# Kernel tuning notes

Measured on AMD Instinct MI355X. Metric: run time of the kernel, lower is better.

Reference implementation:

```python
import jax, jax.numpy as jnp
import numpy as np

NUM_AA, EMB_DIM = 20, 16
H1, H2 = 128, 128
K, EXCLUDE = 64, 3
R_ON, R_CUT = 10.0, 12.0
RBF_CENTERS = (5.0, 6.0, 7.0, 8.0, 9.0, 10.0, 11.0)
RBF_WIDTH = 0.5
M = len(RBF_CENTERS)


def setup_inputs() -> dict:
    key = jax.random.key(0)
    ks = jax.random.split(key, 10)
    B, L = 8, 2048
    R = jax.random.normal(ks[0], (B, L, 3), dtype=jnp.float32) * 10.0  # spread distances over RBF range
    seq = jax.random.randint(ks[1], (B, L), 0, NUM_AA)
    emb_table = jax.random.normal(ks[2], (NUM_AA, EMB_DIM), dtype=jnp.float32) * 0.1
    in_dim = 3 * EMB_DIM
    W1 = jax.random.normal(ks[3], (in_dim, H1), dtype=jnp.float32) / np.sqrt(in_dim)
    b1 = jnp.zeros((H1,), jnp.float32)
    W2 = jax.random.normal(ks[4], (H1, H2), dtype=jnp.float32) / np.sqrt(H1)
    b2 = jnp.zeros((H2,), jnp.float32)
    W3 = jax.random.normal(ks[5], (H2, M), dtype=jnp.float32) / np.sqrt(H2)
    b3 = jnp.zeros((M,), jnp.float32)
    centers = jnp.asarray(RBF_CENTERS, jnp.float32)
    widths = jnp.full((M,), RBF_WIDTH, jnp.float32)
    return {"R": R, "seq": seq, "emb_table": emb_table,
            "W1": W1, "b1": b1, "W2": W2, "b2": b2, "W3": W3, "b3": b3,
            "centers": centers, "widths": widths}


def topk_nonbonded_pairs(R, K, exclude):
    # R: (B, L, 3) -> r: (B, L, K) distances, j: (B, L, K) neighbor indices
    B, L, _ = R.shape
    diff = R[:, :, None, :] - R[:, None, :, :]            # (B, L, L, 3)
    D = jnp.sqrt(jnp.sum(diff * diff, axis=-1) + 1e-12)   # (B, L, L)
    idx = jnp.arange(L)
    bonded = jnp.abs(idx[:, None] - idx[None, :]) <= exclude  # excludes self too
    D = jnp.where(bonded[None], jnp.inf, D)
    neg, j = jax.lax.top_k(-D, K)                          # K smallest distances
    return -neg, j


def smooth_switch(r, r_on, r_cut):
    t = jnp.clip((r - r_on) / (r_cut - r_on), 0.0, 1.0)
    return 1.0 - t * t * (3.0 - 2.0 * t)  # smoothstep down: 1 below r_on, 0 above r_cut


def distance_features(r, centers, widths):
    d = r[..., None] - centers  # (B, L, K, M)
    return jnp.exp(-(d * d) / (2.0 * widths * widths))


def reference(R, seq, emb_table, W1, b1, W2, b2, W3, b3, centers, widths):
    e = emb_table[seq]                                     # (B, L, d)
    r, j = topk_nonbonded_pairs(R, K, EXCLUDE)             # (B, L, K)
    e_j = jnp.take_along_axis(e[:, :, None, :], j[..., None], axis=1)  # wrong axis semantics avoided below
    # gather neighbor embeddings: e_j[b, i, k] = e[b, j[b, i, k]]
    e_j = jnp.take_along_axis(e[:, None, :, :].repeat(1, axis=1), j[..., None], axis=2) if False else \
          jnp.take_along_axis(e[:, :, None, :].transpose(0, 2, 1, 3).repeat(1, axis=0), j[..., None], axis=2) if False else \
          jax.vmap(lambda eb, jb: eb[jb])(e, j)            # (B, L, K, d)
    e_i = jnp.broadcast_to(e[:, :, None, :], e_j.shape)
    pair_feat = jnp.concatenate([e_i, e_j, e_i * e_j], axis=-1)  # (B, L, K, 3d)
    h = jax.nn.relu(pair_feat @ W1 + b1)
    h = jax.nn.relu(h @ W2 + b2)
    w = jax.nn.softplus(h @ W3 + b3)                       # (B, L, K, M)
    phi = distance_features(r, centers, widths)            # (B, L, K, M)
    att = -jnp.sum(w * phi, axis=-1)                       # (B, L, K)
    sw = smooth_switch(r, R_ON, R_CUT)
    return jnp.sum(att * sw, axis=(1, 2))                  # (B,)
```

## Files before the change

kernel.cpp:

```cpp
#include <hip/hip_runtime.h>
#include <math.h>

#define LSEQ 2048
#define KNB 64
#define BATCH 8
#define MRBF 7
#define NTILES 8192
#define NBLOCKS 768
#define BSCALE (255.0f/144.0f)

typedef __attribute__((ext_vector_type(8))) short short8;
typedef __attribute__((ext_vector_type(4))) float floatx4;

__device__ __forceinline__ unsigned short f2bf(float f) {
    unsigned u = __float_as_uint(f);
    u += 0x7fffu + ((u >> 16) & 1u);
    return (unsigned short)(u >> 16);
}
__device__ __forceinline__ unsigned pkbf(float a, float b) {
    return __builtin_amdgcn_perm(__float_as_uint(b) + 0x8000u,
                                 __float_as_uint(a) + 0x8000u, 0x07060302u);
}

__global__ __launch_bounds__(256, 3) void fused_kernel(
    const float* __restrict__ R, const int* __restrict__ seq,
    const float* __restrict__ emb,
    const float* __restrict__ W1, const float* __restrict__ b1,
    const float* __restrict__ W2, const float* __restrict__ b2,
    const float* __restrict__ W3, const float* __restrict__ b3,
    const float* __restrict__ centers, const float* __restrict__ widths,
    float* __restrict__ out)
{
    __shared__ __align__(16) unsigned short lds[24576];
    unsigned short* H1s = lds;
    unsigned short* Xs  = lds + 16384;
    unsigned short* H2s = lds + 8192;
    int*      nbrL    = (int*)lds;
    unsigned* hist    = (unsigned*)((char*)lds + 512);
    float*    cand_d2 = (float*)((char*)lds + 2560);
    int*      cand_j  = (int*)((char*)lds + 3584);
    int*      tctr    = (int*)((char*)lds + 4608);
    int* sB    = tctr + 0;
    int* sNeed = tctr + 2;
    int* oPos  = tctr + 4;
    int* cCnt  = tctr + 6;
    int* fCnt  = tctr + 8;
    __shared__ float bacc[BATCH];

    const int tid  = threadIdx.x;
    const int lane = tid & 63;
    const int wv   = tid >> 6;
    const int l15  = lane & 15;
    const int q    = lane >> 4;

    short8 w1f[2][2], w2f[2][4], w3f[4];
    float b1v[2][4], b2v[2][4];
    #pragma unroll
    for (int mtl = 0; mtl < 2; mtl++) {
        int m = (2*wv + mtl)*16 + l15;
        #pragma unroll
        for (int d = 0; d < 4; d++) {
            b1v[mtl][d] = b1[(2*wv + mtl)*16 + q*4 + d];
            b2v[mtl][d] = b2[(2*wv + mtl)*16 + q*4 + d];
        }
        #pragma unroll
        for (int kt = 0; kt < 2; kt++)
            #pragma unroll
            for (int jj = 0; jj < 8; jj++) {
                int k = kt*32 + q*8 + jj;
                w1f[mtl][kt][jj] = (short)((k < 48) ? f2bf(W1[k*128 + m]) : 0);
            }
        #pragma unroll
        for (int kt = 0; kt < 4; kt++)
            #pragma unroll
            for (int jj = 0; jj < 8; jj++) {
                int k = kt*32 + q*8 + jj;
                w2f[mtl][kt][jj] = (short)f2bf(W2[k*128 + m]);
            }
    }
    #pragma unroll
    for (int kt = 0; kt < 4; kt++)
        #pragma unroll
        for (int jj = 0; jj < 8; jj++) {
            int k = kt*32 + q*8 + jj;
            w3f[kt][jj] = (short)((l15 < MRBF) ? f2bf(W3[k*MRBF + l15]) : 0);
        }
    float b3C[4], cen[4], i2w[4];
    #pragma unroll
    for (int d = 0; d < 4; d++) {
        int rb = q*4 + d;
        bool ok = rb < MRBF;
        b3C[d] = ok ? b3[rb] : 0.f;
        cen[d] = ok ? centers[rb] : 0.f;
        float wd = ok ? widths[rb] : 1.f;
        i2w[d] = 0.5f / (wd*wd);
    }
    if (tid < BATCH) bacc[tid] = 0.f;

    const int pl = tid >> 1, half = tid & 1;
    const int s7p = pl & 7;
    float rloc = 0.f;

    for (int tile = blockIdx.x; tile < NTILES; tile += NBLOCKS) {
        const int b     = tile >> 10;
        const int ibase = (tile & 1023) << 1;
        const float* Rb = R + ((b << 11) * 3);

        __syncthreads();

        hist[tid] = 0u; hist[tid + 256] = 0u;
        if (tid < 2) { oPos[tid] = 0; cCnt[tid] = 0; fCnt[tid] = 0; }

        float px[8], py[8], pz[8];
        {
            const float4* rp = (const float4*)(Rb + tid*24);
            float4 f0=rp[0], f1=rp[1], f2=rp[2], f3=rp[3], f4=rp[4], f5=rp[5];
            px[0]=f0.x; py[0]=f0.y; pz[0]=f0.z;
            px[1]=f0.w; py[1]=f1.x; pz[1]=f1.y;
            px[2]=f1.z; py[2]=f1.w; pz[2]=f2.x;
            px[3]=f2.y; py[3]=f2.z; pz[3]=f2.w;
            px[4]=f3.x; py[4]=f3.y; pz[4]=f3.z;
            px[5]=f3.w; py[5]=f4.x; pz[5]=f4.y;
            px[6]=f4.z; py[6]=f4.w; pz[6]=f5.x;
            px[7]=f5.y; py[7]=f5.z; pz[7]=f5.w;
        }
        float cx0 = Rb[3*ibase+0], cy0 = Rb[3*ibase+1], cz0 = Rb[3*ibase+2];
        float cx1 = Rb[3*ibase+3], cy1 = Rb[3*ibase+4], cz1 = Rb[3*ibase+5];
        __syncthreads();

        float d2r[2][8];
        #pragma unroll
        for (int u = 0; u < 8; u++) {
            int j = tid*8 + u;
            #pragma unroll
            for (int c = 0; c < 2; c++) {
                float dx = (c ? cx1 : cx0) - px[u];
                float dy = (c ? cy1 : cy0) - py[u];
                float dz = (c ? cz1 : cz0) - pz[u];
                float d2 = dx*dx + dy*dy + dz*dz;
                int dd = j - (ibase + c); dd = dd < 0 ? -dd : dd;
                if (dd <= 3) d2 = 1e30f;
                d2r[c][u] = d2;
                if (d2 < 144.0f)
                    atomicAdd(&hist[(c<<8) + (int)(d2*BSCALE)], 1u);
            }
        }
        __syncthreads();

        if (wv < 2) {
            unsigned h4[4]; unsigned s = 0;
            #pragma unroll
            for (int v = 0; v < 4; v++) { h4[v] = hist[(wv<<8) + lane*4 + v]; s += h4[v]; }
            unsigned inc = s;
            #pragma unroll
            for (int off = 1; off < 64; off <<= 1) {
                unsigned n = __shfl_up(inc, off, 64);
                if (lane >= off) inc += n;
            }
            unsigned tot = __shfl(inc, 63, 64);
            unsigned excl = inc - s;
            if (tot < 64u) {
                if (lane == 0) { sB[wv] = 255; sNeed[wv] = 64 - (int)tot; }
            } else if (excl < 64u && 64u <= inc) {
                unsigned cc = excl;
                #pragma unroll
                for (int v = 0; v < 4; v++) {
                    if (cc < 64u && 64u <= cc + h4[v]) { sB[wv] = lane*4+v; sNeed[wv] = 64 - (int)cc; }
                    cc += h4[v];
                }
            }
        }
        __syncthreads();

        #pragma unroll
        for (int u = 0; u < 8; u++) {
            int j = tid*8 + u;
            #pragma unroll
            for (int c = 0; c < 2; c++) {
                float d2 = d2r[c][u];
                int B = sB[c];
                if (d2 < 144.0f) {
                    int key = (int)(d2*BSCALE);
                    if (key < B) {
                        int pos = atomicAdd(&oPos[c], 1);
                        nbrL[(c<<6) + pos] = j;
                    } else if (key == B) {
                        int cc = atomicAdd(&cCnt[c], 1);
                        if (cc < 128) { cand_d2[(c<<7)+cc] = d2; cand_j[(c<<7)+cc] = j; }
                    }
                } else if (B == 255 && d2 < 1e29f) {
                    int t = atomicAdd(&fCnt[c], 1);
                    if (t < sNeed[c]) {
                        int pos = atomicAdd(&oPos[c], 1);
                        nbrL[(c<<6) + pos] = j;
                    }
                }
            }
        }
        __syncthreads();

        if (wv < 2) {
            int B = sB[wv];
            if (B != 255) {
                int cn = cCnt[wv]; if (cn > 128) cn = 128;
                int need = sNeed[wv];
                for (int ci = lane; ci < cn; ci += 64) {
                    float dv = cand_d2[(wv<<7)+ci]; int jv = cand_j[(wv<<7)+ci];
                    int rank = 0;
                    for (int x = 0; x < cn; x++) {
                        float dx2 = cand_d2[(wv<<7)+x]; int jx2 = cand_j[(wv<<7)+x];
                        rank += (dx2 < dv) || (dx2 == dv && jx2 < jv);
                    }
                    if (rank < need) {
                        int pos = atomicAdd(&oPos[wv], 1);
                        nbrL[(wv<<6) + pos] = jv;
                    }
                }
            }
        }
        __syncthreads();

        {
            int c  = pl >> 6;
            int bi = (b << 11) + ibase + c;
            int j  = nbrL[pl];
            int rowj = (b << 11) + j;
            int si = seq[bi], sj = seq[rowj];
            const float4* ei = (const float4*)(emb + si*16 + half*8);
            const float4* ej = (const float4*)(emb + sj*16 + half*8);
            float4 eA0 = ei[0], eA1 = ei[1], eB0 = ej[0], eB1 = ej[1];
            int rb = pl*64;
            uint4 vA = make_uint4(pkbf(eA0.x,eA0.y), pkbf(eA0.z,eA0.w),
                                  pkbf(eA1.x,eA1.y), pkbf(eA1.z,eA1.w));
            uint4 vB = make_uint4(pkbf(eB0.x,eB0.y), pkbf(eB0.z,eB0.w),
                                  pkbf(eB1.x,eB1.y), pkbf(eB1.z,eB1.w));
            uint4 vP = make_uint4(pkbf(eA0.x*eB0.x, eA0.y*eB0.y),
                                  pkbf(eA0.z*eB0.z, eA0.w*eB0.w),
                                  pkbf(eA1.x*eB1.x, eA1.y*eB1.y),
                                  pkbf(eA1.z*eB1.z, eA1.w*eB1.w));
            *(uint4*)&Xs[rb + (((0|half)^s7p)<<3)] = vA;
            *(uint4*)&Xs[rb + (((2|half)^s7p)<<3)] = vB;
            *(uint4*)&Xs[rb + (((4|half)^s7p)<<3)] = vP;
            *(uint4*)&Xs[rb + (((6|half)^s7p)<<3)] = make_uint4(0u,0u,0u,0u);
            if (!half) {
                float dx = R[bi*3+0]-R[rowj*3+0];
                float dy = R[bi*3+1]-R[rowj*3+1];
                float dz = R[bi*3+2]-R[rowj*3+2];
                rloc = sqrtf(dx*dx + dy*dy + dz*dz + 1e-12f);
            }
        }
        __syncthreads();

        #pragma unroll
        for (int nt = 0; nt < 8; nt++) {
            int row = nt*16 + l15;
            int s7 = l15 & 7;
            const unsigned short* xr = Xs + row*64;
            short8 x0 = *(const short8*)&xr[(( q    ^ s7) << 3)];
            short8 x1 = *(const short8*)&xr[(((4|q) ^ s7) << 3)];
            #pragma unroll
            for (int mtl = 0; mtl < 2; mtl++) {
                floatx4 acc = {b1v[mtl][0], b1v[mtl][1], b1v[mtl][2], b1v[mtl][3]};
                acc = __builtin_amdgcn_mfma_f32_16x16x32_bf16(w1f[mtl][0], x0, acc, 0, 0, 0);
                acc = __builtin_amdgcn_mfma_f32_16x16x32_bf16(w1f[mtl][1], x1, acc, 0, 0, 0);
                int chnk = (((2*wv + mtl)*2 + (q>>1)) ^ s7);
                *(uint2*)&H1s[row*128 + (chnk<<3) + ((q&1)<<2)] =
                    make_uint2(pkbf(fmaxf(acc[0],0.f), fmaxf(acc[1],0.f)),
                               pkbf(fmaxf(acc[2],0.f), fmaxf(acc[3],0.f)));
            }
        }
        __syncthreads();

        #pragma unroll
        for (int nt = 4; nt < 8; nt++) {
            int row = nt*16 + l15;
            int s7 = l15 & 7;
            const unsigned short* hr = H1s + row*128;
            short8 hf0 = *(const short8*)&hr[(( q     ^ s7) << 3)];
            short8 hf1 = *(const short8*)&hr[((( 4|q) ^ s7) << 3)];
            short8 hf2 = *(const short8*)&hr[((( 8|q) ^ s7) << 3)];
            short8 hf3 = *(const short8*)&hr[(((12|q) ^ s7) << 3)];
            #pragma unroll
            for (int mtl = 0; mtl < 2; mtl++) {
                floatx4 acc = {b2v[mtl][0], b2v[mtl][1], b2v[mtl][2], b2v[mtl][3]};
                acc = __builtin_amdgcn_mfma_f32_16x16x32_bf16(w2f[mtl][0], hf0, acc, 0, 0, 0);
                acc = __builtin_amdgcn_mfma_f32_16x16x32_bf16(w2f[mtl][1], hf1, acc, 0, 0, 0);
                acc = __builtin_amdgcn_mfma_f32_16x16x32_bf16(w2f[mtl][2], hf2, acc, 0, 0, 0);
                acc = __builtin_amdgcn_mfma_f32_16x16x32_bf16(w2f[mtl][3], hf3, acc, 0, 0, 0);
                int chnk = (((2*wv + mtl)*2 + (q>>1)) ^ s7);
                *(uint2*)&H2s[row*128 + (chnk<<3) + ((q&1)<<2)] =
                    make_uint2(pkbf(fmaxf(acc[0],0.f), fmaxf(acc[1],0.f)),
                               pkbf(fmaxf(acc[2],0.f), fmaxf(acc[3],0.f)));
            }
        }
        __syncthreads();
        #pragma unroll
        for (int nt = 0; nt < 4; nt++) {
            int row = nt*16 + l15;
            int s7 = l15 & 7;
            const unsigned short* hr = H1s + row*128;
            short8 hf0 = *(const short8*)&hr[(( q     ^ s7) << 3)];
            short8 hf1 = *(const short8*)&hr[((( 4|q) ^ s7) << 3)];
            short8 hf2 = *(const short8*)&hr[((( 8|q) ^ s7) << 3)];
            short8 hf3 = *(const short8*)&hr[(((12|q) ^ s7) << 3)];
            #pragma unroll
            for (int mtl = 0; mtl < 2; mtl++) {
                floatx4 acc = {b2v[mtl][0], b2v[mtl][1], b2v[mtl][2], b2v[mtl][3]};
                acc = __builtin_amdgcn_mfma_f32_16x16x32_bf16(w2f[mtl][0], hf0, acc, 0, 0, 0);
                acc = __builtin_amdgcn_mfma_f32_16x16x32_bf16(w2f[mtl][1], hf1, acc, 0, 0, 0);
                acc = __builtin_amdgcn_mfma_f32_16x16x32_bf16(w2f[mtl][2], hf2, acc, 0, 0, 0);
                acc = __builtin_amdgcn_mfma_f32_16x16x32_bf16(w2f[mtl][3], hf3, acc, 0, 0, 0);
                int chnk = (((2*wv + mtl)*2 + (q>>1)) ^ s7);
                *(uint2*)&H2s[row*128 + (chnk<<3) + ((q&1)<<2)] =
                    make_uint2(pkbf(fmaxf(acc[0],0.f), fmaxf(acc[1],0.f)),
                               pkbf(fmaxf(acc[2],0.f), fmaxf(acc[3],0.f)));
            }
        }
        __syncthreads();

        float esum = 0.f;
        #pragma unroll
        for (int ntl = 0; ntl < 2; ntl++) {
            int nt = 2*wv + ntl;
            int row = nt*16 + l15;
            int s7 = l15 & 7;
            const unsigned short* hr = H2s + row*128;
            floatx4 a3 = {b3C[0], b3C[1], b3C[2], b3C[3]};
            #pragma unroll
            for (int kt = 0; kt < 4; kt++) {
                short8 hf = *(const short8*)&hr[((((kt<<2)|q) ^ s7) << 3)];
                a3 = __builtin_amdgcn_mfma_f32_16x16x32_bf16(w3f[kt], hf, a3, 0, 0, 0);
            }
            float rr = __shfl(rloc, (ntl<<5) + 2*l15, 64);
            if (rr < 12.0f) {
                float att = 0.f;
                #pragma unroll
                for (int d = 0; d < 4; d++) {
                    if (q*4 + d < MRBF) {
                        float x = a3[d];
                        float sp = fmaxf(x, 0.f) + __logf(1.f + __expf(-fabsf(x)));
                        float df = rr - cen[d];
                        att += sp * __expf(-df*df*i2w[d]);
                    }
                }
                att += __shfl_xor(att, 16, 64);
                att += __shfl_xor(att, 32, 64);
                float t = fminf(fmaxf((rr - 10.f)*0.5f, 0.f), 1.f);
                float sw = 1.f - t*t*(3.f - 2.f*t);
                esum -= att * sw;
            }
        }
        #pragma unroll
        for (int off = 1; off < 64; off <<= 1)
            esum += __shfl_xor(esum, off, 64);
        if (lane == 0) atomicAdd(&bacc[b], esum * 0.25f);
    }
    __syncthreads();
    if (tid < BATCH) atomicAdd(&out[tid], bacc[tid]);
}

extern "C" void kernel_launch(void* const* d_in, const int* in_sizes, int n_in,
                              void* d_out, int out_size, void* d_ws, size_t ws_size,
                              hipStream_t stream) {
    const float* R       = (const float*)d_in[0];
    const int*   seq     = (const int*)  d_in[1];
    const float* emb     = (const float*)d_in[2];
    const float* W1      = (const float*)d_in[3];
    const float* b1      = (const float*)d_in[4];
    const float* W2      = (const float*)d_in[5];
    const float* b2      = (const float*)d_in[6];
    const float* W3      = (const float*)d_in[7];
    const float* b3      = (const float*)d_in[8];
    const float* centers = (const float*)d_in[9];
    const float* widths  = (const float*)d_in[10];
    float* out = (float*)d_out;

    hipMemsetAsync(d_out, 0, out_size * sizeof(float), stream);

    fused_kernel<<<NBLOCKS, 256, 0, stream>>>(R, seq, emb, W1, b1, W2, b2, W3, b3,
                                              centers, widths, out);
}
```

Measured before the change: 241.3 us.

## Software-pipeline next tile's top-k selection with current tile's MLP stages

Moves the top-k scratch (histogram, candidates, neighbor list) into a separate LDS buffer so it no longer aliases the MLP activation buffers. The neighbor selection for the next tile is then interleaved with the MLP layers of the current tile, sharing existing barriers, so the distance and atomic work can overlap MFMA work and fewer block-wide syncs are needed. Occupancy hint drops from 3 to 2 blocks per CU to cover the extra live registers (d2r carried across stages) and the added LDS.

```diff
diff --git a/kernel.cpp b/kernel.cpp
--- a/kernel.cpp
+++ b/kernel.cpp
@@ -22,7 +22,7 @@
                                  __float_as_uint(a) + 0x8000u, 0x07060302u);
 }
 
-__global__ __launch_bounds__(256, 3) void fused_kernel(
+__global__ __launch_bounds__(256, 2) void fused_kernel(
     const float* __restrict__ R, const int* __restrict__ seq,
     const float* __restrict__ emb,
     const float* __restrict__ W1, const float* __restrict__ b1,
@@ -32,14 +32,15 @@
     float* __restrict__ out)
 {
     __shared__ __align__(16) unsigned short lds[24576];
+    __shared__ __align__(16) unsigned char tkscr[4656];
     unsigned short* H1s = lds;
     unsigned short* Xs  = lds + 16384;
     unsigned short* H2s = lds + 8192;
-    int*      nbrL    = (int*)lds;
-    unsigned* hist    = (unsigned*)((char*)lds + 512);
-    float*    cand_d2 = (float*)((char*)lds + 2560);
-    int*      cand_j  = (int*)((char*)lds + 3584);
-    int*      tctr    = (int*)((char*)lds + 4608);
+    int*      nbrL    = (int*)tkscr;
+    unsigned* hist    = (unsigned*)(tkscr + 512);
+    float*    cand_d2 = (float*)(tkscr + 2560);
+    int*      cand_j  = (int*)(tkscr + 3584);
+    int*      tctr    = (int*)(tkscr + 4608);
     int* sB    = tctr + 0;
     int* sNeed = tctr + 2;
     int* oPos  = tctr + 4;
@@ -100,17 +101,14 @@
     const int pl = tid >> 1, half = tid & 1;
     const int s7p = pl & 7;
     float rloc = 0.f;
-
-    for (int tile = blockIdx.x; tile < NTILES; tile += NBLOCKS) {
-        const int b     = tile >> 10;
-        const int ibase = (tile & 1023) << 1;
-        const float* Rb = R + ((b << 11) * 3);
-
-        __syncthreads();
-
+    float d2r[2][8];
+
+    auto topk_zero = [&]() {
         hist[tid] = 0u; hist[tid + 256] = 0u;
         if (tid < 2) { oPos[tid] = 0; cCnt[tid] = 0; fCnt[tid] = 0; }
-
+    };
+    auto topk_pass1 = [&](int b_, int ibase_) {
+        const float* Rb = R + ((b_ << 11) * 3);
         float px[8], py[8], pz[8];
         {
             const float4* rp = (const float4*)(Rb + tid*24);
@@ -124,11 +122,8 @@
             px[6]=f4.z; py[6]=f4.w; pz[6]=f5.x;
             px[7]=f5.y; py[7]=f5.z; pz[7]=f5.w;
         }
-        float cx0 = Rb[3*ibase+0], cy0 = Rb[3*ibase+1], cz0 = Rb[3*ibase+2];
-        float cx1 = Rb[3*ibase+3], cy1 = Rb[3*ibase+4], cz1 = Rb[3*ibase+5];
-        __syncthreads();
-
-        float d2r[2][8];
+        float cx0 = Rb[3*ibase_+0], cy0 = Rb[3*ibase_+1], cz0 = Rb[3*ibase_+2];
+        float cx1 = Rb[3*ibase_+3], cy1 = Rb[3*ibase_+4], cz1 = Rb[3*ibase_+5];
         #pragma unroll
         for (int u = 0; u < 8; u++) {
             int j = tid*8 + u;
@@ -138,15 +133,15 @@
                 float dy = (c ? cy1 : cy0) - py[u];
                 float dz = (c ? cz1 : cz0) - pz[u];
                 float d2 = dx*dx + dy*dy + dz*dz;
-                int dd = j - (ibase + c); dd = dd < 0 ? -dd : dd;
+                int dd = j - (ibase_ + c); dd = dd < 0 ? -dd : dd;
                 if (dd <= 3) d2 = 1e30f;
                 d2r[c][u] = d2;
                 if (d2 < 144.0f)
                     atomicAdd(&hist[(c<<8) + (int)(d2*BSCALE)], 1u);
             }
         }
-        __syncthreads();
-
+    };
+    auto topk_scan = [&]() {
         if (wv < 2) {
             unsigned h4[4]; unsigned s = 0;
             #pragma unroll
@@ -170,8 +165,8 @@
                 }
             }
         }
-        __syncthreads();
-
+    };
+    auto topk_pass2 = [&]() {
         #pragma unroll
         for (int u = 0; u < 8; u++) {
             int j = tid*8 + u;
@@ -197,8 +192,8 @@
                 }
             }
         }
-        __syncthreads();
-
+    };
+    auto topk_rank = [&]() {
         if (wv < 2) {
             int B = sB[wv];
             if (B != 255) {
@@ -218,39 +213,62 @@
                 }
             }
         }
-        __syncthreads();
-
-        {
-            int c  = pl >> 6;
-            int bi = (b << 11) + ibase + c;
-            int j  = nbrL[pl];
-            int rowj = (b << 11) + j;
-            int si = seq[bi], sj = seq[rowj];
-            const float4* ei = (const float4*)(emb + si*16 + half*8);
-            const float4* ej = (const float4*)(emb + sj*16 + half*8);
-            float4 eA0 = ei[0], eA1 = ei[1], eB0 = ej[0], eB1 = ej[1];
-            int rb = pl*64;
-            uint4 vA = make_uint4(pkbf(eA0.x,eA0.y), pkbf(eA0.z,eA0.w),
-                                  pkbf(eA1.x,eA1.y), pkbf(eA1.z,eA1.w));
-            uint4 vB = make_uint4(pkbf(eB0.x,eB0.y), pkbf(eB0.z,eB0.w),
-                                  pkbf(eB1.x,eB1.y), pkbf(eB1.z,eB1.w));
-            uint4 vP = make_uint4(pkbf(eA0.x*eB0.x, eA0.y*eB0.y),
-                                  pkbf(eA0.z*eB0.z, eA0.w*eB0.w),
-                                  pkbf(eA1.x*eB1.x, eA1.y*eB1.y),
-                                  pkbf(eA1.z*eB1.z, eA1.w*eB1.w));
-            *(uint4*)&Xs[rb + (((0|half)^s7p)<<3)] = vA;
-            *(uint4*)&Xs[rb + (((2|half)^s7p)<<3)] = vB;
-            *(uint4*)&Xs[rb + (((4|half)^s7p)<<3)] = vP;
-            *(uint4*)&Xs[rb + (((6|half)^s7p)<<3)] = make_uint4(0u,0u,0u,0u);
-            if (!half) {
-                float dx = R[bi*3+0]-R[rowj*3+0];
-                float dy = R[bi*3+1]-R[rowj*3+1];
-                float dz = R[bi*3+2]-R[rowj*3+2];
-                rloc = sqrtf(dx*dx + dy*dy + dz*dz + 1e-12f);
-            }
-        }
-        __syncthreads();
-
+    };
+    auto xbuild = [&](int b_, int ibase_) {
+        int c  = pl >> 6;
+        int bi = (b_ << 11) + ibase_ + c;
+        int j  = nbrL[pl];
+        int rowj = (b_ << 11) + j;
+        int si = seq[bi], sj = seq[rowj];
+        const float4* ei = (const float4*)(emb + si*16 + half*8);
+        const float4* ej = (const float4*)(emb + sj*16 + half*8);
+        float4 eA0 = ei[0], eA1 = ei[1], eB0 = ej[0], eB1 = ej[1];
+        int rb = pl*64;
+        uint4 vA = make_uint4(pkbf(eA0.x,eA0.y), pkbf(eA0.z,eA0.w),
+                              pkbf(eA1.x,eA1.y), pkbf(eA1.z,eA1.w));
+        uint4 vB = make_uint4(pkbf(eB0.x,eB0.y), pkbf(eB0.z,eB0.w),
+                              pkbf(eB1.x,eB1.y), pkbf(eB1.z,eB1.w));
+        uint4 vP = make_uint4(pkbf(eA0.x*eB0.x, eA0.y*eB0.y),
+                              pkbf(eA0.z*eB0.z, eA0.w*eB0.w),
+                              pkbf(eA1.x*eB1.x, eA1.y*eB1.y),
+                              pkbf(eA1.z*eB1.z, eA1.w*eB1.w));
+        *(uint4*)&Xs[rb + (((0|half)^s7p)<<3)] = vA;
+        *(uint4*)&Xs[rb + (((2|half)^s7p)<<3)] = vB;
+        *(uint4*)&Xs[rb + (((4|half)^s7p)<<3)] = vP;
+        *(uint4*)&Xs[rb + (((6|half)^s7p)<<3)] = make_uint4(0u,0u,0u,0u);
+        if (!half) {
+            float dx = R[bi*3+0]-R[rowj*3+0];
+            float dy = R[bi*3+1]-R[rowj*3+1];
+            float dz = R[bi*3+2]-R[rowj*3+2];
+            rloc = sqrtf(dx*dx + dy*dy + dz*dz + 1e-12f);
+        }
+    };
+
+    {
+        const int t0 = blockIdx.x;
+        const int b0 = t0 >> 10, i0 = (t0 & 1023) << 1;
+        topk_zero();
+        __syncthreads();
+        topk_pass1(b0, i0);
+        __syncthreads();
+        topk_scan();
+        __syncthreads();
+        topk_pass2();
+        __syncthreads();
+        topk_rank();
+        __syncthreads();
+        xbuild(b0, i0);
+        topk_zero();
+        __syncthreads();
+    }
+
+    for (int t = blockIdx.x; t < NTILES; t += NBLOCKS) {
+        const int b_c = t >> 10;
+        const int nxt = t + NBLOCKS;
+        const bool hn = nxt < NTILES;
+        const int b_n = nxt >> 10, i_n = (nxt & 1023) << 1;
+
+        if (hn) topk_pass1(b_n, i_n);
         #pragma unroll
         for (int nt = 0; nt < 8; nt++) {
             int row = nt*16 + l15;
@@ -271,6 +289,7 @@
         }
         __syncthreads();
 
+        if (hn) topk_scan();
         #pragma unroll
         for (int nt = 4; nt < 8; nt++) {
             int row = nt*16 + l15;
@@ -294,6 +313,8 @@
             }
         }
         __syncthreads();
+
+        if (hn) topk_pass2();
         #pragma unroll
         for (int nt = 0; nt < 4; nt++) {
             int row = nt*16 + l15;
@@ -318,44 +339,54 @@
         }
         __syncthreads();
 
-        float esum = 0.f;
-        #pragma unroll
-        for (int ntl = 0; ntl < 2; ntl++) {
-            int nt = 2*wv + ntl;
-            int row = nt*16 + l15;
-            int s7 = l15 & 7;
-            const unsigned short* hr = H2s + row*128;
-            floatx4 a3 = {b3C[0], b3C[1], b3C[2], b3C[3]};
-            #pragma unroll
-            for (int kt = 0; kt < 4; kt++) {
-                short8 hf = *(const short8*)&hr[((((kt<<2)|q) ^ s7) << 3)];
-                a3 = __builtin_amdgcn_mfma_f32_16x16x32_bf16(w3f[kt], hf, a3, 0, 0, 0);
-            }
-            float rr = __shfl(rloc, (ntl<<5) + 2*l15, 64);
-            if (rr < 12.0f) {
-                float att = 0.f;
+        if (hn) topk_rank();
+        {
+            float esum = 0.f;
+            #pragma unroll
+            for (int ntl = 0; ntl < 2; ntl++) {
+                int nt = 2*wv + ntl;
+                int row = nt*16 + l15;
+                int s7 = l15 & 7;
+                const unsigned short* hr = H2s + row*128;
+                floatx4 a3 = {b3C[0], b3C[1], b3C[2], b3C[3]};
                 #pragma unroll
-                for (int d = 0; d < 4; d++) {
-                    if (q*4 + d < MRBF) {
-                        float x = a3[d];
-                        float sp = fmaxf(x, 0.f) + __logf(1.f + __expf(-fabsf(x)));
-                        float df = rr - cen[d];
-                        att += sp * __expf(-df*df*i2w[d]);
+                for (int kt = 0; kt < 4; kt++) {
+                    short8 hf = *(const short8*)&hr[((((kt<<2)|q) ^ s7) << 3)];
+                    a3 = __builtin_amdgcn_mfma_f32_16x16x32_bf16(w3f[kt], hf, a3, 0, 0, 0);
+                }
+                float rr = __shfl(rloc, (ntl<<5) + 2*l15, 64);
+                if (rr < 12.0f) {
+                    float att = 0.f;
+                    #pragma unroll
+                    for (int d = 0; d < 4; d++) {
+                        if (q*4 + d < MRBF) {
+                            float x = a3[d];
+                            float sp = fmaxf(x, 0.f) + __logf(1.f + __expf(-fabsf(x)));
+                            float df = rr - cen[d];
+                            att += sp * __expf(-df*df*i2w[d]);
+                        }
                     }
+                    att += __shfl_xor(att, 16, 64);
+                    att += __shfl_xor(att, 32, 64);
+                    float tt = fminf(fmaxf((rr - 10.f)*0.5f, 0.f), 1.f);
+                    float sw = 1.f - tt*tt*(3.f - 2.f*tt);
+                    esum -= att * sw;
                 }
-                att += __shfl_xor(att, 16, 64);
-                att += __shfl_xor(att, 32, 64);
-                float t = fminf(fmaxf((rr - 10.f)*0.5f, 0.f), 1.f);
-                float sw = 1.f - t*t*(3.f - 2.f*t);
-                esum -= att * sw;
-            }
-        }
-        #pragma unroll
-        for (int off = 1; off < 64; off <<= 1)
-            esum += __shfl_xor(esum, off, 64);
-        if (lane == 0) atomicAdd(&bacc[b], esum * 0.25f);
+            }
+            #pragma unroll
+            for (int off = 1; off < 64; off <<= 1)
+                esum += __shfl_xor(esum, off, 64);
+            if (lane == 0) atomicAdd(&bacc[b_c], esum * 0.25f);
+        }
+        __syncthreads();
+
+        if (hn) {
+            xbuild(b_n, i_n);
+            topk_zero();
+        }
+        __syncthreads();
     }
-    __syncthreads();
+
     if (tid < BATCH) atomicAdd(&out[tid], bacc[tid]);
 }
 
```

After: 291.2 us. 1.21x slower.

## Compute top-k threshold redundantly per wave and remove per-tile barriers

Applied to the files above, without the earlier changes.

Every wave now runs the histogram prefix scan for both rows itself and broadcasts the threshold bin through a ballot and shuffle, instead of two waves scanning and writing it to shared memory. This removes one barrier and the shared threshold variables. The histogram and counter reset moves to the end of the previous tile, which drops the two barriers at the top of the loop. Launch bounds go from 3 to 2 waves per SIMD, giving the compiler more registers at the cost of occupancy. All waves now do redundant scan work.

```diff
diff --git a/kernel.cpp b/kernel.cpp
--- a/kernel.cpp
+++ b/kernel.cpp
@@ -22,7 +22,7 @@
                                  __float_as_uint(a) + 0x8000u, 0x07060302u);
 }
 
-__global__ __launch_bounds__(256, 3) void fused_kernel(
+__global__ __launch_bounds__(256, 2) void fused_kernel(
     const float* __restrict__ R, const int* __restrict__ seq,
     const float* __restrict__ emb,
     const float* __restrict__ W1, const float* __restrict__ b1,
@@ -40,11 +40,9 @@
     float*    cand_d2 = (float*)((char*)lds + 2560);
     int*      cand_j  = (int*)((char*)lds + 3584);
     int*      tctr    = (int*)((char*)lds + 4608);
-    int* sB    = tctr + 0;
-    int* sNeed = tctr + 2;
-    int* oPos  = tctr + 4;
-    int* cCnt  = tctr + 6;
-    int* fCnt  = tctr + 8;
+    int* oPos  = tctr + 0;
+    int* cCnt  = tctr + 2;
+    int* fCnt  = tctr + 4;
     __shared__ float bacc[BATCH];
 
     const int tid  = threadIdx.x;
@@ -95,21 +93,20 @@
         float wd = ok ? widths[rb] : 1.f;
         i2w[d] = 0.5f / (wd*wd);
     }
-    if (tid < BATCH) bacc[tid] = 0.f;
 
     const int pl = tid >> 1, half = tid & 1;
     const int s7p = pl & 7;
     float rloc = 0.f;
+
+    if (tid < BATCH) bacc[tid] = 0.f;
+    hist[tid] = 0u; hist[tid + 256] = 0u;
+    if (tid < 2) { oPos[tid] = 0; cCnt[tid] = 0; fCnt[tid] = 0; }
+    __syncthreads();
 
     for (int tile = blockIdx.x; tile < NTILES; tile += NBLOCKS) {
         const int b     = tile >> 10;
         const int ibase = (tile & 1023) << 1;
         const float* Rb = R + ((b << 11) * 3);
-
-        __syncthreads();
-
-        hist[tid] = 0u; hist[tid + 256] = 0u;
-        if (tid < 2) { oPos[tid] = 0; cCnt[tid] = 0; fCnt[tid] = 0; }
 
         float px[8], py[8], pz[8];
         {
@@ -126,7 +123,6 @@
         }
         float cx0 = Rb[3*ibase+0], cy0 = Rb[3*ibase+1], cz0 = Rb[3*ibase+2];
         float cx1 = Rb[3*ibase+3], cy1 = Rb[3*ibase+4], cz1 = Rb[3*ibase+5];
-        __syncthreads();
 
         float d2r[2][8];
         #pragma unroll
@@ -147,10 +143,11 @@
         }
         __syncthreads();
 
-        if (wv < 2) {
-            unsigned h4[4]; unsigned s = 0;
-            #pragma unroll
-            for (int v = 0; v < 4; v++) { h4[v] = hist[(wv<<8) + lane*4 + v]; s += h4[v]; }
+        int sBr[2], sNr[2];
+        #pragma unroll
+        for (int c = 0; c < 2; c++) {
+            uint4 hv = *(const uint4*)&hist[(c<<8) + lane*4];
+            unsigned s = hv.x + hv.y + hv.z + hv.w;
             unsigned inc = s;
             #pragma unroll
             for (int off = 1; off < 64; off <<= 1) {
@@ -158,19 +155,28 @@
                 if (lane >= off) inc += n;
             }
             unsigned tot = __shfl(inc, 63, 64);
-            unsigned excl = inc - s;
             if (tot < 64u) {
-                if (lane == 0) { sB[wv] = 255; sNeed[wv] = 64 - (int)tot; }
-            } else if (excl < 64u && 64u <= inc) {
-                unsigned cc = excl;
-                #pragma unroll
-                for (int v = 0; v < 4; v++) {
-                    if (cc < 64u && 64u <= cc + h4[v]) { sB[wv] = lane*4+v; sNeed[wv] = 64 - (int)cc; }
-                    cc += h4[v];
+                sBr[c] = 255; sNr[c] = 64 - (int)tot;
+            } else {
+                unsigned excl = inc - s;
+                bool fnd = (excl < 64u) && (64u <= inc);
+                unsigned pk2 = 0u;
+                if (fnd) {
+                    unsigned cc = excl;
+                    unsigned h4a[4] = {hv.x, hv.y, hv.z, hv.w};
+                    #pragma unroll
+                    for (int v = 0; v < 4; v++) {
+                        if (cc < 64u && 64u <= cc + h4a[v])
+                            pk2 = ((unsigned)(lane*4 + v) << 16) | (64u - cc);
+                        cc += h4a[v];
+                    }
                 }
-            }
-        }
-        __syncthreads();
+                unsigned long long mk = __ballot(fnd);
+                int sl = __ffsll((long long)mk) - 1;
+                unsigned r = __shfl(pk2, sl, 64);
+                sBr[c] = (int)(r >> 16); sNr[c] = (int)(r & 0xffffu);
+            }
+        }
 
         #pragma unroll
         for (int u = 0; u < 8; u++) {
@@ -178,7 +184,7 @@
             #pragma unroll
             for (int c = 0; c < 2; c++) {
                 float d2 = d2r[c][u];
-                int B = sB[c];
+                int B = sBr[c];
                 if (d2 < 144.0f) {
                     int key = (int)(d2*BSCALE);
                     if (key < B) {
@@ -190,7 +196,7 @@
                     }
                 } else if (B == 255 && d2 < 1e29f) {
                     int t = atomicAdd(&fCnt[c], 1);
-                    if (t < sNeed[c]) {
+                    if (t < sNr[c]) {
                         int pos = atomicAdd(&oPos[c], 1);
                         nbrL[(c<<6) + pos] = j;
                     }
@@ -200,10 +206,10 @@
         __syncthreads();
 
         if (wv < 2) {
-            int B = sB[wv];
+            int B  = wv ? sBr[1] : sBr[0];
+            int nd = wv ? sNr[1] : sNr[0];
             if (B != 255) {
                 int cn = cCnt[wv]; if (cn > 128) cn = 128;
-                int need = sNeed[wv];
                 for (int ci = lane; ci < cn; ci += 64) {
                     float dv = cand_d2[(wv<<7)+ci]; int jv = cand_j[(wv<<7)+ci];
                     int rank = 0;
@@ -211,7 +217,7 @@
                         float dx2 = cand_d2[(wv<<7)+x]; int jx2 = cand_j[(wv<<7)+x];
                         rank += (dx2 < dv) || (dx2 == dv && jx2 < jv);
                     }
-                    if (rank < need) {
+                    if (rank < nd) {
                         int pos = atomicAdd(&oPos[wv], 1);
                         nbrL[(wv<<6) + pos] = jv;
                     }
@@ -294,6 +300,7 @@
             }
         }
         __syncthreads();
+
         #pragma unroll
         for (int nt = 0; nt < 4; nt++) {
             int row = nt*16 + l15;
@@ -318,6 +325,9 @@
         }
         __syncthreads();
 
+        hist[tid] = 0u; hist[tid + 256] = 0u;
+        if (tid < 2) { oPos[tid] = 0; cCnt[tid] = 0; fCnt[tid] = 0; }
+
         float esum = 0.f;
         #pragma unroll
         for (int ntl = 0; ntl < 2; ntl++) {
@@ -345,8 +355,8 @@
                 }
                 att += __shfl_xor(att, 16, 64);
                 att += __shfl_xor(att, 32, 64);
-                float t = fminf(fmaxf((rr - 10.f)*0.5f, 0.f), 1.f);
-                float sw = 1.f - t*t*(3.f - 2.f*t);
+                float tt = fminf(fmaxf((rr - 10.f)*0.5f, 0.f), 1.f);
+                float sw = 1.f - tt*tt*(3.f - 2.f*tt);
                 esum -= att * sw;
             }
         }
@@ -354,8 +364,8 @@
         for (int off = 1; off < 64; off <<= 1)
             esum += __shfl_xor(esum, off, 64);
         if (lane == 0) atomicAdd(&bacc[b], esum * 0.25f);
+        __syncthreads();
     }
-    __syncthreads();
     if (tid < BATCH) atomicAdd(&out[tid], bacc[tid]);
 }
 
```

Measured after the change: 294.6 us. +22.1%, slower.
